# Performance work log

Measured on AMD Instinct MI355X. Metric: run time of the kernel, lower is better.

The kernel has to match this reference:

```python
import jax, jax.numpy as jnp
import numpy as np

B, C = 32768, 1000
EPS = 1e-6

def setup_inputs() -> dict:
    key = jax.random.key(0)
    k1, k2 = jax.random.split(key)
    # p_tar / p_vlm are probability distributions over C classes
    p_tar = jax.nn.softmax(jax.random.normal(k1, (B, C), dtype=jnp.float32), axis=1)
    p_vlm = jax.nn.softmax(jax.random.normal(k2, (B, C), dtype=jnp.float32), axis=1)
    alpha = jnp.array([0.99], dtype=jnp.float32)  # EMA momentum
    memory_bank = jnp.full((C, C), 1.0 / C, dtype=jnp.float32)  # __init__ state
    return {"p_tar": p_tar, "p_vlm": p_vlm, "alpha": alpha, "memory_bank": memory_bank}

def _uncertainty(p):
    return -p * jnp.log(p + EPS)

def reference(p_tar, p_vlm, alpha, memory_bank):
    n_classes = memory_bank.shape[0]
    norm = 1.0 / jnp.sqrt(jnp.float32(n_classes))
    # --- class_prototype_atten (uses PRE-update memory bank, as in torch) ---
    atten = jax.nn.softmax(jnp.matmul(p_tar, memory_bank.T) * norm, axis=1)  # [B, C]
    p_tar_new = jnp.matmul(atten, memory_bank)  # [B, C]
    # --- update_membank: vectorized per-class masked-mean EMA ---
    y_tar = jnp.argmax(p_tar, axis=1)
    y_vlm = jnp.argmax(p_vlm, axis=1)
    agree = y_tar == y_vlm
    # non-agreeing rows dumped into extra segment n_classes
    seg = jnp.where(agree, y_tar, n_classes)
    sums = jax.ops.segment_sum(p_tar, seg, num_segments=n_classes + 1)[:n_classes]  # [C, C]
    counts = jax.ops.segment_sum(agree.astype(p_tar.dtype), seg, num_segments=n_classes + 1)[:n_classes]  # [C]
    has = counts > 0
    mean = sums / jnp.where(has, counts, 1.0)[:, None]
    a = alpha.reshape(())
    bank_new = jnp.where(has[:, None], a * memory_bank + (1.0 - a) * mean, memory_bank)
    # --- uncertainty_mixing ---
    eu_tar = jnp.exp(-_uncertainty(p_tar_new))
    eu_vlm = jnp.exp(-_uncertainty(p_vlm))
    p_mix = (eu_tar * p_tar_new + eu_vlm * p_vlm) / (eu_tar + eu_vlm)
    return p_mix, bank_new
```

## Files before the change

kernel.cpp:

```cpp
#include <hip/hip_runtime.h>
#include <hip/hip_bf16.h>
#include <cstdint>
#include <cstddef>

#define NROWS 32768
#define NCLS  1000
#define KP    1024
#define NCH   32

typedef unsigned short u16;
typedef __bf16 bf16x8 __attribute__((ext_vector_type(8)));
typedef float  f32x4  __attribute__((ext_vector_type(4)));


__global__ __launch_bounds__(128)
void prep4_bank(const float* __restrict__ bank,
                __hip_bfloat16* __restrict__ M4,
                __hip_bfloat16* __restrict__ MT4) {
  __shared__ float tile[32][33];
  const int tx = blockIdx.x;
  const int ty = blockIdx.y;
  const int t  = threadIdx.x;
  {
    const int r = t >> 2, c0 = (t & 3) * 8;
    const int gj = ty * 32 + r;
    #pragma unroll
    for (int j = 0; j < 8; ++j) {
      const int gk = tx * 32 + c0 + j;
      tile[r][c0 + j] = (gj < NCLS && gk < NCLS) ? bank[gj * NCLS + gk] : 0.0f;
    }
  }
  __syncthreads();
  const int w = t >> 6, lane = t & 63, lr = lane & 15, qq = lane >> 4;
  if (w == 0) {
    #pragma unroll
    for (int s = 0; s < 2; ++s) {
      bf16x8 o;
      #pragma unroll
      for (int j = 0; j < 8; ++j) o[j] = (__bf16)tile[s * 16 + lr][qq * 8 + j];
      *(bf16x8*)((u16*)M4 + ((size_t)(ty * 2 + s) * NCH + tx) * 512 + lane * 8) = o;
    }
  } else {
    #pragma unroll
    for (int s = 0; s < 2; ++s) {
      bf16x8 o;
      #pragma unroll
      for (int j = 0; j < 8; ++j) o[j] = (__bf16)tile[qq * 8 + j][s * 16 + lr];
      *(bf16x8*)((u16*)MT4 + ((size_t)(tx * 2 + s) * NCH + ty) * 512 + lane * 8) = o;
    }
  }
}

__global__ __launch_bounds__(256)
void rows4_kernel(const float* __restrict__ p_tar, const float* __restrict__ p_vlm,
                  __hip_bfloat16* __restrict__ A4,
                  float* __restrict__ sums, float* __restrict__ counts) {
  __shared__ float sT[4][16]; __shared__ int siT[4][16];
  __shared__ float sV[4][16]; __shared__ int siV[4][16];
  const int w = threadIdx.x >> 6, lane = threadIdx.x & 63;
  const int lr = lane & 15, q = lane >> 4;
  const int panel = blockIdx.x;
  const int row   = panel * 16 + lr;
  const float* tr = p_tar + (size_t)row * NCLS;
  const float* vr = p_vlm + (size_t)row * NCLS;
  u16* a4 = (u16*)A4 + (size_t)panel * NCH * 512 + lane * 8;

  float bvT = -1.0f; int biT = 0;
  float bvV = -1.0f; int biV = 0;
  for (int c = w * 8; c < w * 8 + 8; ++c) {
    const int k0 = c * 32 + q * 8;
    float v[8];
    if (k0 < NCLS) {
      float4 x = *(const float4*)(tr + k0);
      float4 y = *(const float4*)(tr + k0 + 4);
      v[0] = x.x; v[1] = x.y; v[2] = x.z; v[3] = x.w;
      v[4] = y.x; v[5] = y.y; v[6] = y.z; v[7] = y.w;
    } else {
      #pragma unroll
      for (int j = 0; j < 8; ++j) v[j] = 0.0f;
    }
    bf16x8 o;
    #pragma unroll
    for (int j = 0; j < 8; ++j) {
      o[j] = (__bf16)v[j];
      if (v[j] > bvT) { bvT = v[j]; biT = k0 + j; }
    }
    *(bf16x8*)(a4 + (size_t)c * 512) = o;
    if (k0 < NCLS) {
      float4 x = *(const float4*)(vr + k0);
      float4 y = *(const float4*)(vr + k0 + 4);
      float u[8] = {x.x, x.y, x.z, x.w, y.x, y.y, y.z, y.w};
      #pragma unroll
      for (int j = 0; j < 8; ++j)
        if (u[j] > bvV) { bvV = u[j]; biV = k0 + j; }
    }
  }
  #pragma unroll
  for (int d = 16; d < 64; d <<= 1) {
    float ov = __shfl_xor(bvT, d); int oi = __shfl_xor(biT, d);
    if (ov > bvT || (ov == bvT && oi < biT)) { bvT = ov; biT = oi; }
    float ov2 = __shfl_xor(bvV, d); int oi2 = __shfl_xor(biV, d);
    if (ov2 > bvV || (ov2 == bvV && oi2 < biV)) { bvV = ov2; biV = oi2; }
  }
  if (q == 0) { sT[w][lr] = bvT; siT[w][lr] = biT; sV[w][lr] = bvV; siV[w][lr] = biV; }
  __syncthreads();
  float cT = sT[0][lr]; int ciT = siT[0][lr];
  float cV = sV[0][lr]; int ciV = siV[0][lr];
  #pragma unroll
  for (int ww = 1; ww < 4; ++ww) {
    float v1 = sT[ww][lr]; if (v1 > cT) { cT = v1; ciT = siT[ww][lr]; }
    float v2 = sV[ww][lr]; if (v2 > cV) { cV = v2; ciV = siV[ww][lr]; }
  }
  if (w == 0) {
    const int ag = (ciT == ciV) ? 1 : 0;
    for (int rr = 0; rr < 16; ++rr) {
      const int agr = __shfl(ag, rr);
      if (agr) {
        const int cls = __shfl(ciT, rr);
        const float* trr = p_tar + (size_t)(panel * 16 + rr) * NCLS;
        for (int k = lane; k < NCLS; k += 64)
          atomicAdd(&sums[(size_t)cls * NCLS + k], trr[k]);
        if (lane == 0) atomicAdd(&counts[cls], 1.0f);
      }
    }
  }
}

template <int WHICH>
__global__ __launch_bounds__(256, 4)
void gemm4(const u16* __restrict__ A4, const u16* __restrict__ B4,
           __hip_bfloat16* __restrict__ E4out, float* __restrict__ rowsum,
           const float* __restrict__ p_vlm, float* __restrict__ mix_out) {
  __shared__ u16 SH[4][4096];
  const int tid  = threadIdx.x;
  const int w    = tid >> 6;
  const int lane = tid & 63;
  const int lr   = lane & 15;
  const int q    = lane >> 4;
  const int L    = blockIdx.x;
  const int xcd  = L & 7;
  const int jj   = L >> 3;
  const int bm   = xcd * 32 + (jj >> 3);
  const int bn   = jj & 7;
  const int wm   = w >> 1;
  const int wn   = w & 1;

  f32x4 acc[4][4] = {};

  const u16* ga[4];
  const u16* gb[4];
  #pragma unroll
  for (int t = 0; t < 4; ++t) {
    ga[t] = A4 + ((size_t)(bm * 8 + wm * 4 + t) * NCH) * 512 + lane * 8;
    gb[t] = B4 + ((size_t)(bn * 8 + wn * 4 + t) * NCH) * 512 + lane * 8;
  }

  #pragma unroll 2
  for (int i = 0; i < NCH; ++i) {
    const size_t kc = (size_t)i * 512;
    bf16x8 af[4], bfr[4];
    #pragma unroll
    for (int t = 0; t < 4; ++t) af[t]  = *(const bf16x8*)(ga[t] + kc);
    #pragma unroll
    for (int t = 0; t < 4; ++t) bfr[t] = *(const bf16x8*)(gb[t] + kc);
    #pragma unroll
    for (int mt = 0; mt < 4; ++mt)
      #pragma unroll
      for (int nt = 0; nt < 4; ++nt)
        acc[mt][nt] = __builtin_amdgcn_mfma_f32_16x16x32_bf16(af[mt], bfr[nt], acc[mt][nt], 0, 0, 0);
  }

  const float NORM = 0.03162277660168379f;
  if (WHICH == 1) {
    u16* ep = &SH[w][0];
    #pragma unroll
    for (int mt = 0; mt < 4; ++mt) {
      float psum[4] = {0.f, 0.f, 0.f, 0.f};
      #pragma unroll
      for (int nt = 0; nt < 4; ++nt) {
        const int gn = bn * 128 + wn * 64 + nt * 16 + lr;
        const int cc = nt >> 1;
        const int q2 = (nt & 1) * 2 + (lr >> 3);
        const int jj2 = lr & 7;
        #pragma unroll
        for (int r = 0; r < 4; ++r) {
          float e = (gn < NCLS) ? __expf(acc[mt][nt][r] * NORM) : 0.0f;
          psum[r] += e;
          __hip_bfloat16 h = __float2bfloat16(e);
          ep[(mt * 2 + cc) * 512 + (q2 * 16 + q * 4 + r) * 8 + jj2] = *(u16*)&h;
        }
      }
      #pragma unroll
      for (int r = 0; r < 4; ++r) {
        float s = psum[r];
        s += __shfl_xor(s, 1); s += __shfl_xor(s, 2);
        s += __shfl_xor(s, 4); s += __shfl_xor(s, 8);
        if (lr == 0) atomicAdd(&rowsum[bm * 128 + wm * 64 + mt * 16 + q * 4 + r], s);
      }
    }
    #pragma unroll
    for (int ch = 0; ch < 8; ++ch) {
      const int mt = ch >> 1, cc = ch & 1;
      bf16x8 v = *(const bf16x8*)(&ep[ch * 512 + lane * 8]);
      const size_t Rg = bm * 8 + wm * 4 + mt;
      const size_t cg = bn * 4 + wn * 2 + cc;
      *(bf16x8*)((u16*)E4out + (Rg * NCH + cg) * 512 + lane * 8) = v;
    }
  } else {
    #pragma unroll
    for (int mt = 0; mt < 4; ++mt) {
      #pragma unroll
      for (int r = 0; r < 4; ++r) {
        const int gm = bm * 128 + wm * 64 + mt * 16 + q * 4 + r;
        const float inv = 1.0f / rowsum[gm];
        #pragma unroll
        for (int nt = 0; nt < 4; ++nt) {
          const int gn = bn * 128 + wn * 64 + nt * 16 + lr;
          if (gn < NCLS) {
            float pt = acc[mt][nt][r] * inv;
            float pv = p_vlm[(size_t)gm * NCLS + gn];
            float lt = pt * __logf(pt + 1e-6f);
            float lv = pv * __logf(pv + 1e-6f);
            float rr = __expf(lv - lt);
            mix_out[(size_t)gm * NCLS + gn] = (pt + rr * pv) / (1.0f + rr);
          }
        }
      }
    }
  }
}

__global__ __launch_bounds__(256)
void bank_update(const float* __restrict__ bank, const float* __restrict__ sums,
                 const float* __restrict__ counts, const float* __restrict__ alpha,
                 float* __restrict__ out) {
  const int idx = blockIdx.x * 256 + threadIdx.x;
  if (idx >= NCLS * NCLS) return;
  const int r = idx / NCLS;
  const float cnt = counts[r];
  const float bv  = bank[idx];
  const float a   = alpha[0];
  out[idx] = (cnt > 0.0f) ? a * bv + (1.0f - a) * (sums[idx] / cnt) : bv;
}

extern "C" void kernel_launch(void* const* d_in, const int* in_sizes, int n_in,
                              void* d_out, int out_size, void* d_ws, size_t ws_size,
                              hipStream_t stream) {
  const float* p_tar = (const float*)d_in[0];
  const float* p_vlm = (const float*)d_in[1];
  const float* alpha = (const float*)d_in[2];
  const float* bank  = (const float*)d_in[3];
  float* out_mix  = (float*)d_out;
  float* out_bank = (float*)d_out + (size_t)NROWS * NCLS;

  char* w = (char*)d_ws;
  __hip_bfloat16* A4  = (__hip_bfloat16*)w; w += (size_t)NROWS * KP * 2;
  __hip_bfloat16* E4  = (__hip_bfloat16*)w; w += (size_t)NROWS * KP * 2;
  __hip_bfloat16* M4  = (__hip_bfloat16*)w; w += (size_t)KP * KP * 2;
  __hip_bfloat16* MT4 = (__hip_bfloat16*)w; w += (size_t)KP * KP * 2;
  float* sums   = (float*)w;                w += (size_t)NCLS * NCLS * 4;
  float* counts = (float*)w;                w += 1024 * 4;
  float* rs     = (float*)w;                w += (size_t)NROWS * 4;

  hipMemsetAsync(sums, 0, (size_t)NCLS * NCLS * 4 + 1024 * 4 + (size_t)NROWS * 4, stream);

  prep4_bank<<<dim3(32, 32), 128, 0, stream>>>(bank, M4, MT4);
  rows4_kernel<<<NROWS / 16, 256, 0, stream>>>(p_tar, p_vlm, A4, sums, counts);
  gemm4<1><<<2048, 256, 0, stream>>>(
      (const u16*)A4, (const u16*)M4, E4, rs, nullptr, nullptr);
  gemm4<2><<<2048, 256, 0, stream>>>(
      (const u16*)E4, (const u16*)MT4, nullptr, rs, p_vlm, out_mix);
  bank_update<<<(NCLS * NCLS + 255) / 256, 256, 0, stream>>>(bank, sums, counts, alpha, out_bank);
}
```

Baseline: 649.7 us.

## Stage GEMM tiles through LDS with async double-buffered loads and larger blocks

Replaces the direct global-to-register GEMM with a 256x256-tile, 8-wave kernel. A and B chunks are streamed into double-buffered LDS using global_load_lds, so each tile is shared across waves instead of every wave reloading its own fragments from global memory. Barriers and s_setprio are interleaved around the MFMA phases to overlap loads with compute. This cuts global/L2 traffic per FLOP, at the cost of more barriers, higher register pressure (8x4 accumulators) and only 512 blocks.

```diff
diff --git a/kernel.cpp b/kernel.cpp
--- a/kernel.cpp
+++ b/kernel.cpp
@@ -7,11 +7,18 @@
 #define NCLS  1000
 #define KP    1024
 #define NCH   32
+#define NT    32
 
 typedef unsigned short u16;
 typedef __bf16 bf16x8 __attribute__((ext_vector_type(8)));
 typedef float  f32x4  __attribute__((ext_vector_type(4)));
 
+
+__device__ __forceinline__ void gld_lds16(const u16* g, u16* l) {
+  __builtin_amdgcn_global_load_lds(
+      (const __attribute__((address_space(1))) unsigned int*)g,
+      (__attribute__((address_space(3))) unsigned int*)l, 16, 0, 0);
+}
 
 __global__ __launch_bounds__(128)
 void prep4_bank(const float* __restrict__ bank,
@@ -127,95 +134,148 @@
 }
 
 template <int WHICH>
-__global__ __launch_bounds__(256, 4)
-void gemm4(const u16* __restrict__ A4, const u16* __restrict__ B4,
+__global__ __launch_bounds__(512, 2)
+void gemm8(const u16* __restrict__ A4, const u16* __restrict__ B4,
            __hip_bfloat16* __restrict__ E4out, float* __restrict__ rowsum,
            const float* __restrict__ p_vlm, float* __restrict__ mix_out) {
-  __shared__ u16 SH[4][4096];
+  __shared__ u16 SH[32768];
   const int tid  = threadIdx.x;
   const int w    = tid >> 6;
   const int lane = tid & 63;
   const int lr   = lane & 15;
   const int q    = lane >> 4;
+  const int wr   = w >> 2;
+  const int wc   = w & 3;
   const int L    = blockIdx.x;
   const int xcd  = L & 7;
-  const int jj   = L >> 3;
-  const int bm   = xcd * 32 + (jj >> 3);
-  const int bn   = jj & 7;
-  const int wm   = w >> 1;
-  const int wn   = w & 1;
-
-  f32x4 acc[4][4] = {};
-
-  const u16* ga[4];
-  const u16* gb[4];
-  #pragma unroll
-  for (int t = 0; t < 4; ++t) {
-    ga[t] = A4 + ((size_t)(bm * 8 + wm * 4 + t) * NCH) * 512 + lane * 8;
-    gb[t] = B4 + ((size_t)(bn * 8 + wn * 4 + t) * NCH) * 512 + lane * 8;
-  }
-
-  #pragma unroll 2
-  for (int i = 0; i < NCH; ++i) {
-    const size_t kc = (size_t)i * 512;
+  const int j    = L >> 3;
+  const int bm   = xcd * 16 + (j >> 2);
+  const int bn   = j & 3;
+
+  f32x4 acc[8][4] = {};
+
+  const u16* gA0 = A4 + ((size_t)(bm * 16 + w)     * NCH) * 512 + lane * 8;
+  const u16* gA1 = A4 + ((size_t)(bm * 16 + w + 8) * NCH) * 512 + lane * 8;
+  const u16* gB0 = B4 + ((size_t)(bn * 16 + w)     * NCH) * 512 + lane * 8;
+  const u16* gB1 = B4 + ((size_t)(bn * 16 + w + 8) * NCH) * 512 + lane * 8;
+
+  #define STAGE_A(t, s)                                         \
+    do { const size_t ko = (size_t)(t) * 512;                   \
+      gld_lds16(gA0 + ko, SH + (s) * 8192 + w * 512);           \
+      gld_lds16(gA1 + ko, SH + (s) * 8192 + (w + 8) * 512);     \
+    } while (0)
+  #define STAGE_B(t, s)                                         \
+    do { const size_t ko = (size_t)(t) * 512;                   \
+      gld_lds16(gB0 + ko, SH + 16384 + (s) * 8192 + w * 512);   \
+      gld_lds16(gB1 + ko, SH + 16384 + (s) * 8192 + (w + 8) * 512); \
+    } while (0)
+
+  STAGE_A(0, 0);
+  STAGE_B(0, 0);
+
+  for (int t = 0; t < NT; ++t) {
+    const int s = t & 1, ns = s ^ 1;
+    if (t + 1 < NT) {
+      STAGE_A(t + 1, ns);
+      asm volatile("s_waitcnt vmcnt(2)" ::: "memory");
+    } else {
+      asm volatile("s_waitcnt vmcnt(0)" ::: "memory");
+    }
+    __builtin_amdgcn_s_barrier();
+    asm volatile("" ::: "memory");
+    const u16* sA = SH + s * 8192;
+    const u16* sB = SH + 16384 + s * 8192;
     bf16x8 af[4], bfr[4];
     #pragma unroll
-    for (int t = 0; t < 4; ++t) af[t]  = *(const bf16x8*)(ga[t] + kc);
-    #pragma unroll
-    for (int t = 0; t < 4; ++t) bfr[t] = *(const bf16x8*)(gb[t] + kc);
+    for (int nt = 0; nt < 4; ++nt)
+      bfr[nt] = *(const bf16x8*)(sB + (wc * 4 + nt) * 512 + lane * 8);
+    #pragma unroll
+    for (int mt = 0; mt < 4; ++mt)
+      af[mt] = *(const bf16x8*)(sA + (wr * 8 + mt) * 512 + lane * 8);
+    if (t + 1 < NT) STAGE_B(t + 1, ns);
+    asm volatile("" ::: "memory");
+    __builtin_amdgcn_s_barrier();
+    asm volatile("" ::: "memory");
+    __builtin_amdgcn_s_setprio(1);
     #pragma unroll
     for (int mt = 0; mt < 4; ++mt)
       #pragma unroll
       for (int nt = 0; nt < 4; ++nt)
         acc[mt][nt] = __builtin_amdgcn_mfma_f32_16x16x32_bf16(af[mt], bfr[nt], acc[mt][nt], 0, 0, 0);
-  }
-
+    __builtin_amdgcn_s_setprio(0);
+    asm volatile("" ::: "memory");
+    __builtin_amdgcn_s_barrier();
+    asm volatile("" ::: "memory");
+    bf16x8 af2[4];
+    #pragma unroll
+    for (int mt = 0; mt < 4; ++mt)
+      af2[mt] = *(const bf16x8*)(sA + (wr * 8 + 4 + mt) * 512 + lane * 8);
+    asm volatile("" ::: "memory");
+    __builtin_amdgcn_s_barrier();
+    asm volatile("" ::: "memory");
+    __builtin_amdgcn_s_setprio(1);
+    #pragma unroll
+    for (int mt = 0; mt < 4; ++mt)
+      #pragma unroll
+      for (int nt = 0; nt < 4; ++nt)
+        acc[4 + mt][nt] = __builtin_amdgcn_mfma_f32_16x16x32_bf16(af2[mt], bfr[nt], acc[4 + mt][nt], 0, 0, 0);
+    __builtin_amdgcn_s_setprio(0);
+  }
+  #undef STAGE_A
+  #undef STAGE_B
+
+  __syncthreads();
   const float NORM = 0.03162277660168379f;
   if (WHICH == 1) {
-    u16* ep = &SH[w][0];
-    #pragma unroll
-    for (int mt = 0; mt < 4; ++mt) {
-      float psum[4] = {0.f, 0.f, 0.f, 0.f};
-      #pragma unroll
-      for (int nt = 0; nt < 4; ++nt) {
-        const int gn = bn * 128 + wn * 64 + nt * 16 + lr;
-        const int cc = nt >> 1;
-        const int q2 = (nt & 1) * 2 + (lr >> 3);
-        const int jj2 = lr & 7;
+    u16* ep = SH + w * 4096;
+    #pragma unroll
+    for (int rr2 = 0; rr2 < 2; ++rr2) {
+      #pragma unroll
+      for (int mtl = 0; mtl < 4; ++mtl) {
+        const int mt = rr2 * 4 + mtl;
+        float psum[4] = {0.f, 0.f, 0.f, 0.f};
+        #pragma unroll
+        for (int nt = 0; nt < 4; ++nt) {
+          const int gn = bn * 256 + wc * 64 + nt * 16 + lr;
+          const int cc = nt >> 1;
+          const int q2 = (nt & 1) * 2 + (lr >> 3);
+          const int jj2 = lr & 7;
+          #pragma unroll
+          for (int r = 0; r < 4; ++r) {
+            float e = (gn < NCLS) ? __expf(acc[mt][nt][r] * NORM) : 0.0f;
+            psum[r] += e;
+            __hip_bfloat16 h = __float2bfloat16(e);
+            ep[(mtl * 2 + cc) * 512 + (q2 * 16 + q * 4 + r) * 8 + jj2] = *(u16*)&h;
+          }
+        }
         #pragma unroll
         for (int r = 0; r < 4; ++r) {
-          float e = (gn < NCLS) ? __expf(acc[mt][nt][r] * NORM) : 0.0f;
-          psum[r] += e;
-          __hip_bfloat16 h = __float2bfloat16(e);
-          ep[(mt * 2 + cc) * 512 + (q2 * 16 + q * 4 + r) * 8 + jj2] = *(u16*)&h;
+          float sm = psum[r];
+          sm += __shfl_xor(sm, 1); sm += __shfl_xor(sm, 2);
+          sm += __shfl_xor(sm, 4); sm += __shfl_xor(sm, 8);
+          if (lr == 0)
+            atomicAdd(&rowsum[bm * 256 + wr * 128 + mt * 16 + q * 4 + r], sm);
         }
       }
       #pragma unroll
+      for (int ch = 0; ch < 8; ++ch) {
+        const int mtl = ch >> 1, cc = ch & 1;
+        bf16x8 v = *(const bf16x8*)(ep + ch * 512 + lane * 8);
+        const size_t Rg = bm * 16 + wr * 8 + rr2 * 4 + mtl;
+        const size_t cg = bn * 8 + wc * 2 + cc;
+        *(bf16x8*)((u16*)E4out + (Rg * NCH + cg) * 512 + lane * 8) = v;
+      }
+    }
+  } else {
+    #pragma unroll
+    for (int mt = 0; mt < 8; ++mt) {
+      #pragma unroll
       for (int r = 0; r < 4; ++r) {
-        float s = psum[r];
-        s += __shfl_xor(s, 1); s += __shfl_xor(s, 2);
-        s += __shfl_xor(s, 4); s += __shfl_xor(s, 8);
-        if (lr == 0) atomicAdd(&rowsum[bm * 128 + wm * 64 + mt * 16 + q * 4 + r], s);
-      }
-    }
-    #pragma unroll
-    for (int ch = 0; ch < 8; ++ch) {
-      const int mt = ch >> 1, cc = ch & 1;
-      bf16x8 v = *(const bf16x8*)(&ep[ch * 512 + lane * 8]);
-      const size_t Rg = bm * 8 + wm * 4 + mt;
-      const size_t cg = bn * 4 + wn * 2 + cc;
-      *(bf16x8*)((u16*)E4out + (Rg * NCH + cg) * 512 + lane * 8) = v;
-    }
-  } else {
-    #pragma unroll
-    for (int mt = 0; mt < 4; ++mt) {
-      #pragma unroll
-      for (int r = 0; r < 4; ++r) {
-        const int gm = bm * 128 + wm * 64 + mt * 16 + q * 4 + r;
+        const int gm = bm * 256 + wr * 128 + mt * 16 + q * 4 + r;
         const float inv = 1.0f / rowsum[gm];
         #pragma unroll
         for (int nt = 0; nt < 4; ++nt) {
-          const int gn = bn * 128 + wn * 64 + nt * 16 + lr;
+          const int gn = bn * 256 + wc * 64 + nt * 16 + lr;
           if (gn < NCLS) {
             float pt = acc[mt][nt][r] * inv;
             float pv = p_vlm[(size_t)gm * NCLS + gn];
@@ -266,9 +326,9 @@
 
   prep4_bank<<<dim3(32, 32), 128, 0, stream>>>(bank, M4, MT4);
   rows4_kernel<<<NROWS / 16, 256, 0, stream>>>(p_tar, p_vlm, A4, sums, counts);
-  gemm4<1><<<2048, 256, 0, stream>>>(
+  gemm8<1><<<512, 512, 0, stream>>>(
       (const u16*)A4, (const u16*)M4, E4, rs, nullptr, nullptr);
-  gemm4<2><<<2048, 256, 0, stream>>>(
+  gemm8<2><<<512, 512, 0, stream>>>(
       (const u16*)E4, (const u16*)MT4, nullptr, rs, p_vlm, out_mix);
   bank_update<<<(NCLS * NCLS + 255) / 256, 256, 0, stream>>>(bank, sums, counts, alpha, out_bank);
 }
```

After: 594.9 us. 8.4% less time.
